# Performance work log

Hardware: AMD Instinct MI355X
Metric: run time of the kernel (lower is better)

Reference implementation:

```python
import jax, jax.numpy as jnp
import numpy as np

NHEAD = 8
DILATED = 1


def setup_inputs() -> dict:
    key = jax.random.key(0)
    ks = jax.random.split(key, 5)
    bs, c, h, w, k = 2, 256, 128, 128, 8
    L = (h // 2) * (w // 2)
    return {
        "query": jax.random.normal(ks[0], (bs, c, h, w), jnp.float32),
        "key": jax.random.normal(ks[1], (bs, c, h, w), jnp.float32),
        "value": jax.random.normal(ks[2], (bs, c, h, w), jnp.float32),
        "topk_pos": jax.random.randint(ks[3], (bs, L, k, 2), 0, h // 2, dtype=jnp.int32).astype(jnp.int64),
        "rel_pos": jax.random.normal(ks[4], (bs, NHEAD, h, w, 4 * k), jnp.float32),
    }


def reference(query, key, value, topk_pos, rel_pos):
    bs, c, h0, w0 = query.shape
    h1, w1 = key.shape[2], key.shape[3]
    nh = NHEAD
    d = c // nh
    L = (h0 // 2) * (w0 // 2)
    k = topk_pos.shape[2]
    k4 = 4 * k

    # key/value: [b,c,h,w] -> [b, h1*w1, nh, d]
    kf = key.reshape(bs, c, h1 * w1).transpose(0, 2, 1).reshape(bs, h1 * w1, nh, d)
    vf = value.reshape(bs, c, h1 * w1).transpose(0, 2, 1).reshape(bs, h1 * w1, nh, d)

    # query grouped into 2x2 blocks: [b, L, 4, nh, d]
    q = query.reshape(bs, nh, d, h0 // 2, 2, w0 // 2, 2)
    q = q.transpose(0, 3, 5, 4, 6, 1, 2).reshape(bs, L, 4, nh, d)

    # build gather indices into flattened key grid (offsets by dilation)
    tp = topk_pos * 2                               # [b, L, k, 2]
    row, col = tp[..., 0], tp[..., 1]
    offs = [(0, 0), (0, DILATED), (DILATED, 0), (DILATED, DILATED)]
    idx = jnp.stack([(row + x) * w1 + (col + y) for x, y in offs], axis=3)  # [b,L,k,4]
    idx = jnp.clip(idx, 0, h1 * w1 - 1).reshape(bs, L, k4)

    def gather(tbl):  # tbl: [b, h1*w1, nh, d] -> [b, L, k4, nh, d]
        return jax.vmap(lambda t, i: t[i])(tbl, idx.reshape(bs, L * k4)).reshape(bs, L, k4, nh, d)

    kg = gather(kf)
    vg = gather(vf)

    scale = 1.0 / np.sqrt(d).astype(np.float32)
    qk = jnp.einsum('blthd,blmhd->bltmh', q, kg) * scale  # [b,L,4,k4,nh]

    rp = rel_pos.reshape(bs, nh, h0 // 2, 2, w0 // 2, 2, k4)
    rp = rp.transpose(0, 2, 4, 3, 5, 6, 1).reshape(bs, L, 4, k4, nh)
    qk = qk + rp

    A = jax.nn.softmax(qk, axis=-2)  # softmax over the k*4 candidate axis
    msg = jnp.einsum('bltmh,blmhd->blthd', A, vg)  # [b,L,4,nh,d]

    # un-group 2x2 blocks back to full resolution: [b, h0*w0, c]
    msg = msg.reshape(bs, h0 // 2, w0 // 2, 2, 2, nh, d)
    msg = msg.transpose(0, 1, 3, 2, 4, 5, 6).reshape(bs, h0 * w0, c)

    up_idx = jnp.broadcast_to(idx[:, :, None, :], (bs, L, 4, k4))
    up_idx = up_idx.reshape(bs, h0 // 2, w0 // 2, 2, 2, k4)
    up_idx = up_idx.transpose(0, 1, 3, 2, 4, 5).reshape(bs, h0 * w0, k4)
    return msg, up_idx
```

## Files before the change

### kernel.cpp

```cpp
#include <hip/hip_runtime.h>
#include <hip/hip_fp16.h>
#include <math.h>

constexpr int NH = 8;
constexpr int D = 32;
constexpr int C = 256;
constexpr int H0 = 128;
constexpr int W0 = 128;
constexpr int PIX = H0 * W0;
constexpr int LBLK = 4096;
constexpr int K4 = 32;
constexpr int KSTH = 260;
constexpr int KST = 258;

typedef _Float16 half2_t __attribute__((ext_vector_type(2)));

#if defined(__has_builtin)
#if __has_builtin(__builtin_amdgcn_fdot2)
#define HAVE_FDOT2 1
#endif
#endif

__device__ __forceinline__ float fdot2_acc(half2_t a, half2_t b, float c) {
#ifdef HAVE_FDOT2
  return __builtin_amdgcn_fdot2(a, b, c, false);
#else
  return c + (float)a.x * (float)b.x + (float)a.y * (float)b.y;
#endif
}

__global__ __launch_bounds__(256) void transpose_qkv_kernel(
    const float* __restrict__ q, const float* __restrict__ k,
    const float* __restrict__ v, __half* __restrict__ qT,
    __half* __restrict__ kT, __half* __restrict__ vT)
{
  __shared__ float tile[64 * 65];
  const int z = blockIdx.z;
  const int b = z & 1;
  const int arr = z >> 1;
  const float* src = (arr == 0 ? q : arr == 1 ? k : v) + (size_t)b * C * PIX;
  __half* dst = (arr == 0 ? qT : arr == 1 ? kT : vT) + (size_t)b * PIX * C;

  const int p0 = blockIdx.x * 64;
  const int c0 = blockIdx.y * 64;
  const int t15 = threadIdx.x & 15;
  const int thi4 = threadIdx.x >> 4;

#pragma unroll
  for (int r = 0; r < 4; ++r) {
    const int ch = thi4 + r * 16;
    const int p4 = t15 * 4;
    float4 f = *(const float4*)&src[(size_t)(c0 + ch) * PIX + p0 + p4];
    tile[(p4 + 0) * 65 + ch] = f.x;
    tile[(p4 + 1) * 65 + ch] = f.y;
    tile[(p4 + 2) * 65 + ch] = f.z;
    tile[(p4 + 3) * 65 + ch] = f.w;
  }
  __syncthreads();

  const int t7 = threadIdx.x & 7;
  const int th8 = threadIdx.x >> 3;
#pragma unroll
  for (int r = 0; r < 2; ++r) {
    const int p = th8 + r * 32;
    const int c8 = t7 * 8;
    const float* tr = &tile[p * 65 + c8];
    __half2 h0 = __floats2half2_rn(tr[0], tr[1]);
    __half2 h1 = __floats2half2_rn(tr[2], tr[3]);
    __half2 h2 = __floats2half2_rn(tr[4], tr[5]);
    __half2 h3 = __floats2half2_rn(tr[6], tr[7]);
    uint4 u;
    u.x = *(unsigned*)&h0; u.y = *(unsigned*)&h1;
    u.z = *(unsigned*)&h2; u.w = *(unsigned*)&h3;
    *(uint4*)&dst[(size_t)(p0 + p) * C + c0 + c8] = u;
  }
}

__global__ __launch_bounds__(256) void cascade_attn_f16(
    const __half* __restrict__ qT,
    const __half* __restrict__ kT,
    const __half* __restrict__ vT,
    const int* __restrict__ topk,
    const float* __restrict__ relp,
    float* __restrict__ out_msg,
    float* __restrict__ out_idx)
{
  __shared__ __half kvh[K4 * KSTH];
  __shared__ __half qph[4 * C];

  const int tid = threadIdx.x;
  const int bid = blockIdx.x;
  const int b = bid >> 12;
  const int l = bid & (LBLK - 1);
  const int by = l >> 6, bx = l & 63;
  const int r0 = by * 2, c0 = bx * 2;

  const int* tp = topk + ((size_t)b * LBLK + l) * 16;

  const int h = tid >> 5;
  const int m = tid & 31;

  {
    const int t = tid >> 6, ln = tid & 63;
    const int pix = r0 * W0 + c0 + (t >> 1) * W0 + (t & 1);
    uint2 f = *(const uint2*)&qT[((size_t)b * PIX + pix) * C + ln * 4];
    *(uint2*)&qph[t * C + ln * 4] = f;
  }

  const int p = tid >> 3;
  const int ln8 = tid & 7;
  const int jj = p >> 2, po = p & 3;
  const int gpix = (tp[jj * 2] * 2 + (po >> 1)) * W0 + tp[jj * 2 + 1] * 2 + (po & 1);

  {
    const __half* src = &kT[((size_t)b * PIX + gpix) * C + ln8 * 8];
#pragma unroll
    for (int i = 0; i < 4; ++i) {
      uint4 f = *(const uint4*)(src + i * 64);
      __half* dst = &kvh[p * KSTH + ln8 * 8 + i * 64];
      *(uint2*)dst = make_uint2(f.x, f.y);
      *(uint2*)(dst + 4) = make_uint2(f.z, f.w);
    }
  }

  uint4 vreg[4];
  {
    const __half* src = &vT[((size_t)b * PIX + gpix) * C + ln8 * 8];
#pragma unroll
    for (int i = 0; i < 4; ++i) vreg[i] = *(const uint4*)(src + i * 64);
  }

  const size_t rb = ((((size_t)b * NH + h) * H0 + r0) * W0 + c0) * K4 + m;
  float rl0 = relp[rb];
  float rl1 = relp[rb + K4];
  float rl2 = relp[rb + (size_t)W0 * K4];
  float rl3 = relp[rb + (size_t)W0 * K4 + K4];

  if (tid < 128) {
    const int mm = tid & 31, t = tid >> 5;
    const int j2 = mm >> 2, o2 = mm & 3;
    const int pix = (tp[j2 * 2] * 2 + (o2 >> 1)) * W0 + tp[j2 * 2 + 1] * 2 + (o2 & 1);
    const int prow = r0 + (t >> 1), pcol = c0 + (t & 1);
    out_idx[((size_t)b * PIX + prow * W0 + pcol) * K4 + mm] = (float)pix;
  }
  __syncthreads();

  uint2 kw[8];
  {
    const __half* kbase = &kvh[m * KSTH + h * D];
#pragma unroll
    for (int i = 0; i < 8; ++i) kw[i] = *(const uint2*)(kbase + i * 4);
  }
  const half2_t* kh = (const half2_t*)kw;

  float acc[4] = {0.f, 0.f, 0.f, 0.f};
#pragma unroll
  for (int t = 0; t < 4; ++t) {
    uint4 qw[2];
    const uint4* qf = (const uint4*)&qph[t * C + h * D];
    qw[0] = qf[0];
    qw[1] = qf[1];
    const half2_t* qh2 = (const half2_t*)qw;
    uint4 qw2[2];
    qw2[0] = qf[2];
    qw2[1] = qf[3];
    const half2_t* qh2b = (const half2_t*)qw2;
#pragma unroll
    for (int i = 0; i < 8; ++i) acc[t] = fdot2_acc(qh2[i], kh[i], acc[t]);
#pragma unroll
    for (int i = 0; i < 8; ++i) acc[t] = fdot2_acc(qh2b[i], kh[8 + i], acc[t]);
  }

  const float scale = 0.17677669529663687f;
  float sv[4];
  sv[0] = acc[0] * scale + rl0;
  sv[1] = acc[1] * scale + rl1;
  sv[2] = acc[2] * scale + rl2;
  sv[3] = acc[3] * scale + rl3;

  float pr4[4];
#pragma unroll
  for (int t = 0; t < 4; ++t) {
    float x = sv[t];
    float mx = x;
#pragma unroll
    for (int off = 16; off > 0; off >>= 1) mx = fmaxf(mx, __shfl_xor(mx, off));
    float pbit = __expf(x - mx);
    float sm = pbit;
#pragma unroll
    for (int off = 16; off > 0; off >>= 1) sm += __shfl_xor(sm, off);
    pr4[t] = pbit / sm;
  }
  __syncthreads();

  {
    const int d = m >> 1, lohi = m & 1;
#pragma unroll
    for (int t = 0; t < 4; ++t)
      qph[h * 128 + d * 8 + t * 2 + lohi] = __float2half(pr4[t]);
  }
#pragma unroll
  for (int i = 0; i < 4; ++i) {
    __half* dst = &kvh[p * KSTH + ln8 * 8 + i * 64];
    *(uint2*)dst = make_uint2(vreg[i].x, vreg[i].y);
    *(uint2*)(dst + 4) = make_uint2(vreg[i].z, vreg[i].w);
  }
  __syncthreads();

  float o0 = 0.f, o1 = 0.f, o2 = 0.f, o3 = 0.f;
  const uint4* pp = (const uint4*)&qph[h * 128];
  const __half* vcol = &kvh[h * D + m];
#pragma unroll
  for (int d = 0; d < 16; ++d) {
    uint4 u = pp[d];
    __half vlo = vcol[(2 * d) * KSTH];
    __half vhi = vcol[(2 * d + 1) * KSTH];
    __half2 vp2 = __halves2half2(vlo, vhi);
    half2_t vp = __builtin_bit_cast(half2_t, vp2);
    o0 = fdot2_acc(__builtin_bit_cast(half2_t, u.x), vp, o0);
    o1 = fdot2_acc(__builtin_bit_cast(half2_t, u.y), vp, o1);
    o2 = fdot2_acc(__builtin_bit_cast(half2_t, u.z), vp, o2);
    o3 = fdot2_acc(__builtin_bit_cast(half2_t, u.w), vp, o3);
  }

  const size_t ob = ((size_t)b * PIX + (size_t)r0 * W0 + c0) * C + h * D + m;
  out_msg[ob] = o0;
  out_msg[ob + C] = o1;
  out_msg[ob + (size_t)W0 * C] = o2;
  out_msg[ob + (size_t)W0 * C + C] = o3;
}

__global__ __launch_bounds__(256) void cascade_attn_fallback(
    const float* __restrict__ query, const float* __restrict__ key,
    const float* __restrict__ value, const int* __restrict__ topk,
    const float* __restrict__ relp, float* __restrict__ out_msg,
    float* __restrict__ out_idx)
{
  __shared__ float kv[K4 * KST];
  __shared__ float qs[4 * C];
  __shared__ float as_[NH * K4 * 4];

  const int tid = threadIdx.x;
  const int bid = blockIdx.x;
  const int b = bid >> 12;
  const int l = bid & (LBLK - 1);
  const int by = l >> 6, bx = l & 63;
  const int r0 = by * 2, c0 = bx * 2;

  const size_t plane = (size_t)PIX;
  const float* qb = query + (size_t)b * C * plane;
  const float* kb = key + (size_t)b * C * plane;
  const float* vb = value + (size_t)b * C * plane;
  const int* tp = topk + ((size_t)b * LBLK + l) * 16;

  {
    const float* qp = qb + (size_t)tid * plane + r0 * W0 + c0;
    float2 a = *(const float2*)qp;
    float2 bb = *(const float2*)(qp + W0);
    qs[0 * C + tid] = a.x; qs[1 * C + tid] = a.y;
    qs[2 * C + tid] = bb.x; qs[3 * C + tid] = bb.y;
  }
#pragma unroll
  for (int it = 0; it < 16; ++it) {
    const int jj = it >> 1, x = it & 1;
    const int pr = tp[jj * 2] * 2 + x;
    const int pc = tp[jj * 2 + 1] * 2;
    float2 f = *(const float2*)(kb + (size_t)tid * plane + pr * W0 + pc);
    const int m0 = jj * 4 + x * 2;
    kv[m0 * KST + tid] = f.x;
    kv[(m0 + 1) * KST + tid] = f.y;
  }
  if (tid < 128) {
    const int m = tid & 31, t = tid >> 5;
    const int jj = m >> 2, o = m & 3;
    const int pix = (tp[jj * 2] * 2 + (o >> 1)) * W0 + tp[jj * 2 + 1] * 2 + (o & 1);
    const int prow = r0 + (t >> 1), pcol = c0 + (t & 1);
    out_idx[((size_t)b * plane + prow * W0 + pcol) * K4 + m] = (float)pix;
  }
  __syncthreads();

  const int h = tid >> 5;
  const int m = tid & 31;
  float a0 = 0.f, a1 = 0.f, a2 = 0.f, a3 = 0.f;
#pragma unroll
  for (int dq = 0; dq < 8; ++dq) {
    const int off = h * D + dq * 4;
    float4 q0 = *(const float4*)&qs[0 * C + off];
    float4 q1 = *(const float4*)&qs[1 * C + off];
    float4 q2 = *(const float4*)&qs[2 * C + off];
    float4 q3 = *(const float4*)&qs[3 * C + off];
    float2 ka = *(const float2*)&kv[m * KST + off];
    float2 kc = *(const float2*)&kv[m * KST + off + 2];
    a0 += q0.x * ka.x + q0.y * ka.y + q0.z * kc.x + q0.w * kc.y;
    a1 += q1.x * ka.x + q1.y * ka.y + q1.z * kc.x + q1.w * kc.y;
    a2 += q2.x * ka.x + q2.y * ka.y + q2.z * kc.x + q2.w * kc.y;
    a3 += q3.x * ka.x + q3.y * ka.y + q3.z * kc.x + q3.w * kc.y;
  }
  const float scale = 0.17677669529663687f;
  const size_t rb = ((((size_t)b * NH + h) * H0 + r0) * W0 + c0) * K4 + m;
  float sv[4];
  sv[0] = a0 * scale + relp[rb];
  sv[1] = a1 * scale + relp[rb + K4];
  sv[2] = a2 * scale + relp[rb + (size_t)W0 * K4];
  sv[3] = a3 * scale + relp[rb + (size_t)W0 * K4 + K4];
  float pr4[4];
#pragma unroll
  for (int t = 0; t < 4; ++t) {
    float x = sv[t];
    float mx = x;
#pragma unroll
    for (int off = 16; off > 0; off >>= 1) mx = fmaxf(mx, __shfl_xor(mx, off));
    float pbit = __expf(x - mx);
    float sm = pbit;
#pragma unroll
    for (int off = 16; off > 0; off >>= 1) sm += __shfl_xor(sm, off);
    pr4[t] = pbit / sm;
  }
  *(float4*)&as_[tid * 4] = make_float4(pr4[0], pr4[1], pr4[2], pr4[3]);
  __syncthreads();
#pragma unroll
  for (int it = 0; it < 16; ++it) {
    const int jj = it >> 1, x = it & 1;
    const int pr = tp[jj * 2] * 2 + x;
    const int pc = tp[jj * 2 + 1] * 2;
    float2 f = *(const float2*)(vb + (size_t)tid * plane + pr * W0 + pc);
    const int m0 = jj * 4 + x * 2;
    kv[m0 * KST + tid] = f.x;
    kv[(m0 + 1) * KST + tid] = f.y;
  }
  __syncthreads();
  float o0 = 0.f, o1 = 0.f, o2 = 0.f, o3 = 0.f;
#pragma unroll
  for (int mm = 0; mm < 32; ++mm) {
    float4 a4 = *(const float4*)&as_[(h * K4 + mm) * 4];
    float vv = kv[mm * KST + h * D + m];
    o0 += a4.x * vv; o1 += a4.y * vv; o2 += a4.z * vv; o3 += a4.w * vv;
  }
  const size_t ob = ((size_t)b * plane + (size_t)r0 * W0 + c0) * C + h * D + m;
  out_msg[ob] = o0;
  out_msg[ob + C] = o1;
  out_msg[ob + (size_t)W0 * C] = o2;
  out_msg[ob + (size_t)W0 * C + C] = o3;
}

extern "C" void kernel_launch(void* const* d_in, const int* in_sizes, int n_in,
                              void* d_out, int out_size, void* d_ws, size_t ws_size,
                              hipStream_t stream) {
  const float* q = (const float*)d_in[0];
  const float* k = (const float*)d_in[1];
  const float* v = (const float*)d_in[2];
  const int* tp = (const int*)d_in[3];
  const float* rp = (const float*)d_in[4];

  float* out_msg = (float*)d_out;
  float* out_idx = out_msg + (size_t)2 * PIX * C;

  const size_t n_elem = (size_t)2 * PIX * C;
  const size_t needed = 3 * n_elem * sizeof(__half);
  if (ws_size >= needed) {
    __half* qT = (__half*)d_ws;
    __half* kT = qT + n_elem;
    __half* vT = kT + n_elem;
    dim3 tg(PIX / 64, C / 64, 6);
    hipLaunchKernelGGL(transpose_qkv_kernel, tg, dim3(256), 0, stream,
                       q, k, v, qT, kT, vT);
    hipLaunchKernelGGL(cascade_attn_f16, dim3(2 * LBLK), dim3(256), 0, stream,
                       qT, kT, vT, tp, rp, out_msg, out_idx);
  } else {
    hipLaunchKernelGGL(cascade_attn_fallback, dim3(2 * LBLK), dim3(256), 0, stream,
                       q, k, v, tp, rp, out_msg, out_idx);
  }
}
```

Before: 201.4 us.

## Process two query blocks per workgroup with software-pipelined K/Q loads and register V gather

Each workgroup now handles two adjacent 2x2 query blocks, halving the grid. While the first block's softmax and PV run, the second block's K rows and Q are prefetched into registers. V is no longer staged through shared memory: each thread gathers its own column of V values directly into registers as half2 pairs. Probabilities go to a separate shared buffer, which removes one barrier per block. In exchange, register pressure rises and the V gathers become scattered 2-byte global loads.

```diff
diff --git a/kernel.cpp b/kernel.cpp
--- a/kernel.cpp
+++ b/kernel.cpp
@@ -87,33 +87,46 @@
 {
   __shared__ __half kvh[K4 * KSTH];
   __shared__ __half qph[4 * C];
+  __shared__ __half pph[NH * 128];
 
   const int tid = threadIdx.x;
   const int bid = blockIdx.x;
-  const int b = bid >> 12;
-  const int l = bid & (LBLK - 1);
-  const int by = l >> 6, bx = l & 63;
-  const int r0 = by * 2, c0 = bx * 2;
-
-  const int* tp = topk + ((size_t)b * LBLK + l) * 16;
+  const int b = bid >> 11;
+  const int l0 = (bid & 2047) * 2;
+  const int l1 = l0 + 1;
+  const int by = l0 >> 6;
+  const int r0 = by * 2;
+  const int c00 = (l0 & 63) * 2;
+  const int c01 = (l1 & 63) * 2;
+
+  const int* tp0 = topk + ((size_t)b * LBLK + l0) * 16;
+  const int* tp1 = topk + ((size_t)b * LBLK + l1) * 16;
 
   const int h = tid >> 5;
   const int m = tid & 31;
-
-  {
-    const int t = tid >> 6, ln = tid & 63;
-    const int pix = r0 * W0 + c0 + (t >> 1) * W0 + (t & 1);
-    uint2 f = *(const uint2*)&qT[((size_t)b * PIX + pix) * C + ln * 4];
-    *(uint2*)&qph[t * C + ln * 4] = f;
-  }
-
   const int p = tid >> 3;
   const int ln8 = tid & 7;
+
+  int tpl0[16], tpl1[16];
+#pragma unroll
+  for (int i = 0; i < 16; ++i) tpl0[i] = tp0[i];
+#pragma unroll
+  for (int i = 0; i < 16; ++i) tpl1[i] = tp1[i];
+
+  const int qt = tid >> 6, qln = tid & 63;
+  const int qpix0 = r0 * W0 + c00 + (qt >> 1) * W0 + (qt & 1);
+  const int qpix1 = r0 * W0 + c01 + (qt >> 1) * W0 + (qt & 1);
+  {
+    uint2 f = *(const uint2*)&qT[((size_t)b * PIX + qpix0) * C + qln * 4];
+    *(uint2*)&qph[qt * C + qln * 4] = f;
+  }
+  uint2 qld1 = *(const uint2*)&qT[((size_t)b * PIX + qpix1) * C + qln * 4];
+
   const int jj = p >> 2, po = p & 3;
-  const int gpix = (tp[jj * 2] * 2 + (po >> 1)) * W0 + tp[jj * 2 + 1] * 2 + (po & 1);
-
-  {
-    const __half* src = &kT[((size_t)b * PIX + gpix) * C + ln8 * 8];
+  const int gpix0 = (tp0[jj * 2] * 2 + (po >> 1)) * W0 + tp0[jj * 2 + 1] * 2 + (po & 1);
+  const int gpix1 = (tp1[jj * 2] * 2 + (po >> 1)) * W0 + tp1[jj * 2 + 1] * 2 + (po & 1);
+  {
+    const __half* src = &kT[((size_t)b * PIX + gpix0) * C + ln8 * 8];
 #pragma unroll
     for (int i = 0; i < 4; ++i) {
       uint4 f = *(const uint4*)(src + i * 64);
@@ -123,24 +136,32 @@
     }
   }
 
-  uint4 vreg[4];
-  {
-    const __half* src = &vT[((size_t)b * PIX + gpix) * C + ln8 * 8];
-#pragma unroll
-    for (int i = 0; i < 4; ++i) vreg[i] = *(const uint4*)(src + i * 64);
-  }
-
-  const size_t rb = ((((size_t)b * NH + h) * H0 + r0) * W0 + c0) * K4 + m;
-  float rl0 = relp[rb];
-  float rl1 = relp[rb + K4];
-  float rl2 = relp[rb + (size_t)W0 * K4];
-  float rl3 = relp[rb + (size_t)W0 * K4 + K4];
-
-  if (tid < 128) {
-    const int mm = tid & 31, t = tid >> 5;
+  __half2 vp0[16];
+#pragma unroll
+  for (int d = 0; d < 16; ++d) {
+    const int m0 = 2 * d, m1 = 2 * d + 1;
+    const int rr0 = tpl0[(m0 >> 2) * 2] * 2 + ((m0 & 3) >> 1);
+    const int cc0 = tpl0[(m0 >> 2) * 2 + 1] * 2 + (m0 & 1);
+    const int rr1 = tpl0[(m1 >> 2) * 2] * 2 + ((m1 & 3) >> 1);
+    const int cc1 = tpl0[(m1 >> 2) * 2 + 1] * 2 + (m1 & 1);
+    vp0[d] = __halves2half2(vT[((size_t)b * PIX + rr0 * W0 + cc0) * C + h * D + m],
+                            vT[((size_t)b * PIX + rr1 * W0 + cc1) * C + h * D + m]);
+  }
+
+  const size_t rb0 = ((((size_t)b * NH + h) * H0 + r0) * W0 + c00) * K4 + m;
+  float rl0 = relp[rb0];
+  float rl1 = relp[rb0 + K4];
+  float rl2 = relp[rb0 + (size_t)W0 * K4];
+  float rl3 = relp[rb0 + (size_t)W0 * K4 + K4];
+
+  {
+    const int tt = tid & 127;
+    const int mm = tt & 31, t = tt >> 5;
+    const int* tpx = (tid < 128) ? tp0 : tp1;
+    const int c0x = (tid < 128) ? c00 : c01;
     const int j2 = mm >> 2, o2 = mm & 3;
-    const int pix = (tp[j2 * 2] * 2 + (o2 >> 1)) * W0 + tp[j2 * 2 + 1] * 2 + (o2 & 1);
-    const int prow = r0 + (t >> 1), pcol = c0 + (t & 1);
+    const int pix = (tpx[j2 * 2] * 2 + (o2 >> 1)) * W0 + tpx[j2 * 2 + 1] * 2 + (o2 & 1);
+    const int prow = r0 + (t >> 1), pcol = c0x + (t & 1);
     out_idx[((size_t)b * PIX + prow * W0 + pcol) * K4 + mm] = (float)pix;
   }
   __syncthreads();
@@ -151,83 +172,169 @@
 #pragma unroll
     for (int i = 0; i < 8; ++i) kw[i] = *(const uint2*)(kbase + i * 4);
   }
-  const half2_t* kh = (const half2_t*)kw;
-
-  float acc[4] = {0.f, 0.f, 0.f, 0.f};
-#pragma unroll
-  for (int t = 0; t < 4; ++t) {
-    uint4 qw[2];
-    const uint4* qf = (const uint4*)&qph[t * C + h * D];
-    qw[0] = qf[0];
-    qw[1] = qf[1];
-    const half2_t* qh2 = (const half2_t*)qw;
-    uint4 qw2[2];
-    qw2[0] = qf[2];
-    qw2[1] = qf[3];
-    const half2_t* qh2b = (const half2_t*)qw2;
-#pragma unroll
-    for (int i = 0; i < 8; ++i) acc[t] = fdot2_acc(qh2[i], kh[i], acc[t]);
-#pragma unroll
-    for (int i = 0; i < 8; ++i) acc[t] = fdot2_acc(qh2b[i], kh[8 + i], acc[t]);
-  }
-
-  const float scale = 0.17677669529663687f;
-  float sv[4];
-  sv[0] = acc[0] * scale + rl0;
-  sv[1] = acc[1] * scale + rl1;
-  sv[2] = acc[2] * scale + rl2;
-  sv[3] = acc[3] * scale + rl3;
-
-  float pr4[4];
-#pragma unroll
-  for (int t = 0; t < 4; ++t) {
-    float x = sv[t];
-    float mx = x;
-#pragma unroll
-    for (int off = 16; off > 0; off >>= 1) mx = fmaxf(mx, __shfl_xor(mx, off));
-    float pbit = __expf(x - mx);
-    float sm = pbit;
-#pragma unroll
-    for (int off = 16; off > 0; off >>= 1) sm += __shfl_xor(sm, off);
-    pr4[t] = pbit / sm;
-  }
-  __syncthreads();
-
-  {
-    const int d = m >> 1, lohi = m & 1;
+  {
+    const half2_t* kh = (const half2_t*)kw;
+    float acc[4] = {0.f, 0.f, 0.f, 0.f};
+#pragma unroll
+    for (int t = 0; t < 4; ++t) {
+      uint4 qw[2];
+      const uint4* qf = (const uint4*)&qph[t * C + h * D];
+      qw[0] = qf[0]; qw[1] = qf[1];
+      const half2_t* qh2 = (const half2_t*)qw;
+      uint4 qw2[2];
+      qw2[0] = qf[2]; qw2[1] = qf[3];
+      const half2_t* qh2b = (const half2_t*)qw2;
+#pragma unroll
+      for (int i = 0; i < 8; ++i) acc[t] = fdot2_acc(qh2[i], kh[i], acc[t]);
+#pragma unroll
+      for (int i = 0; i < 8; ++i) acc[t] = fdot2_acc(qh2b[i], kh[8 + i], acc[t]);
+    }
+    const float scale = 0.17677669529663687f;
+    float sv[4];
+    sv[0] = acc[0] * scale + rl0;
+    sv[1] = acc[1] * scale + rl1;
+    sv[2] = acc[2] * scale + rl2;
+    sv[3] = acc[3] * scale + rl3;
+    float pr4[4];
+#pragma unroll
+    for (int t = 0; t < 4; ++t) {
+      float x = sv[t];
+      float mx = x;
+#pragma unroll
+      for (int off = 16; off > 0; off >>= 1) mx = fmaxf(mx, __shfl_xor(mx, off));
+      float pbit = __expf(x - mx);
+      float sm = pbit;
+#pragma unroll
+      for (int off = 16; off > 0; off >>= 1) sm += __shfl_xor(sm, off);
+      pr4[t] = pbit / sm;
+    }
+    const int dd = m >> 1, lohi = m & 1;
 #pragma unroll
     for (int t = 0; t < 4; ++t)
-      qph[h * 128 + d * 8 + t * 2 + lohi] = __float2half(pr4[t]);
-  }
+      pph[h * 128 + dd * 8 + t * 2 + lohi] = __float2half(pr4[t]);
+  }
+  __syncthreads();
+
+  uint4 kreg1[4];
+  {
+    const __half* src = &kT[((size_t)b * PIX + gpix1) * C + ln8 * 8];
+#pragma unroll
+    for (int i = 0; i < 4; ++i) kreg1[i] = *(const uint4*)(src + i * 64);
+  }
+
+  {
+    float o0 = 0.f, o1 = 0.f, o2 = 0.f, o3 = 0.f;
+    const uint4* pp = (const uint4*)&pph[h * 128];
+#pragma unroll
+    for (int d = 0; d < 16; ++d) {
+      uint4 u = pp[d];
+      half2_t vp = __builtin_bit_cast(half2_t, vp0[d]);
+      o0 = fdot2_acc(__builtin_bit_cast(half2_t, u.x), vp, o0);
+      o1 = fdot2_acc(__builtin_bit_cast(half2_t, u.y), vp, o1);
+      o2 = fdot2_acc(__builtin_bit_cast(half2_t, u.z), vp, o2);
+      o3 = fdot2_acc(__builtin_bit_cast(half2_t, u.w), vp, o3);
+    }
+    const size_t ob = ((size_t)b * PIX + (size_t)r0 * W0 + c00) * C + h * D + m;
+    out_msg[ob] = o0;
+    out_msg[ob + C] = o1;
+    out_msg[ob + (size_t)W0 * C] = o2;
+    out_msg[ob + (size_t)W0 * C + C] = o3;
+  }
+
+  __half2 vp1[16];
+#pragma unroll
+  for (int d = 0; d < 16; ++d) {
+    const int m0 = 2 * d, m1 = 2 * d + 1;
+    const int rr0 = tpl1[(m0 >> 2) * 2] * 2 + ((m0 & 3) >> 1);
+    const int cc0 = tpl1[(m0 >> 2) * 2 + 1] * 2 + (m0 & 1);
+    const int rr1 = tpl1[(m1 >> 2) * 2] * 2 + ((m1 & 3) >> 1);
+    const int cc1 = tpl1[(m1 >> 2) * 2 + 1] * 2 + (m1 & 1);
+    vp1[d] = __halves2half2(vT[((size_t)b * PIX + rr0 * W0 + cc0) * C + h * D + m],
+                            vT[((size_t)b * PIX + rr1 * W0 + cc1) * C + h * D + m]);
+  }
+
 #pragma unroll
   for (int i = 0; i < 4; ++i) {
     __half* dst = &kvh[p * KSTH + ln8 * 8 + i * 64];
-    *(uint2*)dst = make_uint2(vreg[i].x, vreg[i].y);
-    *(uint2*)(dst + 4) = make_uint2(vreg[i].z, vreg[i].w);
-  }
-  __syncthreads();
-
-  float o0 = 0.f, o1 = 0.f, o2 = 0.f, o3 = 0.f;
-  const uint4* pp = (const uint4*)&qph[h * 128];
-  const __half* vcol = &kvh[h * D + m];
-#pragma unroll
-  for (int d = 0; d < 16; ++d) {
-    uint4 u = pp[d];
-    __half vlo = vcol[(2 * d) * KSTH];
-    __half vhi = vcol[(2 * d + 1) * KSTH];
-    __half2 vp2 = __halves2half2(vlo, vhi);
-    half2_t vp = __builtin_bit_cast(half2_t, vp2);
-    o0 = fdot2_acc(__builtin_bit_cast(half2_t, u.x), vp, o0);
-    o1 = fdot2_acc(__builtin_bit_cast(half2_t, u.y), vp, o1);
-    o2 = fdot2_acc(__builtin_bit_cast(half2_t, u.z), vp, o2);
-    o3 = fdot2_acc(__builtin_bit_cast(half2_t, u.w), vp, o3);
-  }
-
-  const size_t ob = ((size_t)b * PIX + (size_t)r0 * W0 + c0) * C + h * D + m;
-  out_msg[ob] = o0;
-  out_msg[ob + C] = o1;
-  out_msg[ob + (size_t)W0 * C] = o2;
-  out_msg[ob + (size_t)W0 * C + C] = o3;
+    *(uint2*)dst = make_uint2(kreg1[i].x, kreg1[i].y);
+    *(uint2*)(dst + 4) = make_uint2(kreg1[i].z, kreg1[i].w);
+  }
+  *(uint2*)&qph[qt * C + qln * 4] = qld1;
+  __syncthreads();
+
+  const size_t rb1 = ((((size_t)b * NH + h) * H0 + r0) * W0 + c01) * K4 + m;
+  float sl0 = relp[rb1];
+  float sl1 = relp[rb1 + K4];
+  float sl2 = relp[rb1 + (size_t)W0 * K4];
+  float sl3 = relp[rb1 + (size_t)W0 * K4 + K4];
+
+  {
+    const __half* kbase = &kvh[m * KSTH + h * D];
+#pragma unroll
+    for (int i = 0; i < 8; ++i) kw[i] = *(const uint2*)(kbase + i * 4);
+  }
+  {
+    const half2_t* kh = (const half2_t*)kw;
+    float acc[4] = {0.f, 0.f, 0.f, 0.f};
+#pragma unroll
+    for (int t = 0; t < 4; ++t) {
+      uint4 qw[2];
+      const uint4* qf = (const uint4*)&qph[t * C + h * D];
+      qw[0] = qf[0]; qw[1] = qf[1];
+      const half2_t* qh2 = (const half2_t*)qw;
+      uint4 qw2[2];
+      qw2[0] = qf[2]; qw2[1] = qf[3];
+      const half2_t* qh2b = (const half2_t*)qw2;
+#pragma unroll
+      for (int i = 0; i < 8; ++i) acc[t] = fdot2_acc(qh2[i], kh[i], acc[t]);
+#pragma unroll
+      for (int i = 0; i < 8; ++i) acc[t] = fdot2_acc(qh2b[i], kh[8 + i], acc[t]);
+    }
+    const float scale = 0.17677669529663687f;
+    float sv[4];
+    sv[0] = acc[0] * scale + sl0;
+    sv[1] = acc[1] * scale + sl1;
+    sv[2] = acc[2] * scale + sl2;
+    sv[3] = acc[3] * scale + sl3;
+    float pr4[4];
+#pragma unroll
+    for (int t = 0; t < 4; ++t) {
+      float x = sv[t];
+      float mx = x;
+#pragma unroll
+      for (int off = 16; off > 0; off >>= 1) mx = fmaxf(mx, __shfl_xor(mx, off));
+      float pbit = __expf(x - mx);
+      float sm = pbit;
+#pragma unroll
+      for (int off = 16; off > 0; off >>= 1) sm += __shfl_xor(sm, off);
+      pr4[t] = pbit / sm;
+    }
+    const int dd = m >> 1, lohi = m & 1;
+#pragma unroll
+    for (int t = 0; t < 4; ++t)
+      pph[h * 128 + dd * 8 + t * 2 + lohi] = __float2half(pr4[t]);
+  }
+  asm volatile("s_waitcnt lgkmcnt(0)" ::: "memory");
+  __builtin_amdgcn_sched_barrier(0);
+
+  {
+    float o0 = 0.f, o1 = 0.f, o2 = 0.f, o3 = 0.f;
+    const uint4* pp = (const uint4*)&pph[h * 128];
+#pragma unroll
+    for (int d = 0; d < 16; ++d) {
+      uint4 u = pp[d];
+      half2_t vp = __builtin_bit_cast(half2_t, vp1[d]);
+      o0 = fdot2_acc(__builtin_bit_cast(half2_t, u.x), vp, o0);
+      o1 = fdot2_acc(__builtin_bit_cast(half2_t, u.y), vp, o1);
+      o2 = fdot2_acc(__builtin_bit_cast(half2_t, u.z), vp, o2);
+      o3 = fdot2_acc(__builtin_bit_cast(half2_t, u.w), vp, o3);
+    }
+    const size_t ob = ((size_t)b * PIX + (size_t)r0 * W0 + c01) * C + h * D + m;
+    out_msg[ob] = o0;
+    out_msg[ob + C] = o1;
+    out_msg[ob + (size_t)W0 * C] = o2;
+    out_msg[ob + (size_t)W0 * C + C] = o3;
+  }
 }
 
 __global__ __launch_bounds__(256) void cascade_attn_fallback(
@@ -364,7 +471,7 @@
     dim3 tg(PIX / 64, C / 64, 6);
     hipLaunchKernelGGL(transpose_qkv_kernel, tg, dim3(256), 0, stream,
                        q, k, v, qT, kT, vT);
-    hipLaunchKernelGGL(cascade_attn_f16, dim3(2 * LBLK), dim3(256), 0, stream,
+    hipLaunchKernelGGL(cascade_attn_f16, dim3(LBLK), dim3(256), 0, stream,
                        qT, kT, vT, tp, rp, out_msg, out_idx);
   } else {
     hipLaunchKernelGGL(cascade_attn_fallback, dim3(2 * LBLK), dim3(256), 0, stream,
```

Measured after the change: 203.1 us. Within noise of the previous version (+0.8%).
